# Optimization experiments

Hardware: AMD Instinct MI355X
Metric: run time of the kernel (lower is better)

The kernel has to match this reference:

```python
import jax, jax.numpy as jnp
import numpy as np

B, T, DE, DD, A, FN, FS = 32, 2000, 512, 1024, 128, 32, 16
TEMPERATURE = 1.0


def setup_inputs() -> dict:
    key = jax.random.key(0)
    ks = jax.random.split(key, 10)
    input_enc = jax.random.normal(ks[0], (B, T, DE), dtype=jnp.float32)
    # lengths in [T//2, T] so no zero-length utterances
    enc_lengths = jax.random.randint(ks[1], (B,), T // 2, T + 1, dtype=jnp.int32)
    input_dec = jax.random.normal(ks[2], (B, DD), dtype=jnp.float32)
    # prev_att: previous-step attention weights (masked, normalized)
    prev_att = jax.random.uniform(ks[3], (B, T), dtype=jnp.float32)
    pad = jnp.arange(T)[None, :] >= enc_lengths[:, None]
    prev_att = jnp.where(pad, 0.0, prev_att)
    prev_att = prev_att / jnp.sum(prev_att, axis=1, keepdims=True)
    # parameters
    conv_w = jax.random.normal(ks[4], (FN, 1, 2 * FS + 1), dtype=jnp.float32) * 0.1  # [out,in,k]
    enc_w = jax.random.normal(ks[5], (A, DE), dtype=jnp.float32) * 0.04
    dec_w = jax.random.normal(ks[6], (A, DD), dtype=jnp.float32) * 0.03
    att_w = jax.random.normal(ks[7], (A, FN), dtype=jnp.float32) * 0.17
    att_b = jnp.zeros((A,), dtype=jnp.float32)
    out_w = jax.random.normal(ks[8], (1, A), dtype=jnp.float32) * 0.09
    return dict(input_enc=input_enc, enc_lengths=enc_lengths, input_dec=input_dec,
                prev_att=prev_att, conv_w=conv_w, enc_w=enc_w, dec_w=dec_w,
                att_w=att_w, att_b=att_b, out_w=out_w)


def reference(input_enc, enc_lengths, input_dec, prev_att,
              conv_w, enc_w, dec_w, att_w, att_b, out_w):
    b, t, _ = input_enc.shape
    fs = (conv_w.shape[-1] - 1) // 2  # 'same' padding
    # padding mask: True at padded positions t >= length
    mask = jnp.arange(t)[None, :] >= enc_lengths[:, None]  # [B,T]
    # location features: Conv1d over prev attention, 1 -> FN channels, same length
    conv = jax.lax.conv_general_dilated(
        prev_att[:, None, :], conv_w, window_strides=(1,),
        padding=[(fs, fs)], dimension_numbers=("NCH", "OIH", "NCH"))  # [B,FN,T]
    loc_feat = conv.transpose(0, 2, 1)  # [B,T,FN]
    projected_att = loc_feat @ att_w.T + att_b        # [B,T,A]
    projected_enc = input_enc @ enc_w.T               # [B,T,A]
    projected_dec = (input_dec @ dec_w.T)[:, None, :]  # [B,1,A]
    score = jnp.squeeze(jnp.tanh(projected_att + projected_enc + projected_dec) @ out_w.T, -1)  # [B,T]
    score = jnp.where(mask, -jnp.inf, score)
    att_weight = jax.nn.softmax(TEMPERATURE * score, axis=1)  # [B,T]
    context = jnp.einsum("btd,bt->bd", input_enc, att_weight)  # [B,DE]
    return context, att_weight
```

## Files before the change

### kernel.cpp

```cpp
#include <hip/hip_runtime.h>
#include <hip/hip_bf16.h>
#include <math.h>

#define B_ 32
#define T_ 2000
#define DE_ 512
#define DD_ 1024
#define A_ 128
#define FN_ 32
#define FS_ 16
#define KW_ (2*FS_+1)

typedef __bf16 bf16x8 __attribute__((ext_vector_type(8)));
typedef __bf16 bf16x4 __attribute__((ext_vector_type(4)));
typedef float f32x4 __attribute__((ext_vector_type(4)));

#define BT 64
#define LSTR 40

__device__ __forceinline__ void load_lds16(const void* g, void* l) {
    __builtin_amdgcn_global_load_lds(
        (const __attribute__((address_space(1))) unsigned int*)g,
        (__attribute__((address_space(3))) unsigned int*)l, 16, 0, 0);
}

__global__ __launch_bounds__(256) void prep_kernel(
    const float* __restrict__ enc_w, const float* __restrict__ att_w,
    const float* __restrict__ input_dec, const float* __restrict__ dec_w,
    const float* __restrict__ att_b,
    __bf16* __restrict__ enc_bf, __bf16* __restrict__ att_bf,
    float* __restrict__ pdec)
{
    int bx = blockIdx.x, tid = threadIdx.x;
    if (bx < 64) {
        int i = bx * 256 + tid;
        float4 v = ((const float4*)enc_w)[i];
        bf16x4 o;
        o[0] = (__bf16)v.x; o[1] = (__bf16)v.y; o[2] = (__bf16)v.z; o[3] = (__bf16)v.w;
        *(bf16x4*)(enc_bf + (size_t)i * 4) = o;
        if (i < (A_ * FN_) / 4) {
            float4 w = ((const float4*)att_w)[i];
            bf16x4 p;
            p[0] = (__bf16)w.x; p[1] = (__bf16)w.y; p[2] = (__bf16)w.z; p[3] = (__bf16)w.w;
            *(bf16x4*)(att_bf + (size_t)i * 4) = p;
        }
    } else {
        int pb = bx - 64;
        int b  = pb >> 2;
        int a0 = (pb & 3) * 32;
        int al = tid >> 3;
        int kg = tid & 7;
        int a  = a0 + al;
        const float4* w = (const float4*)(dec_w + (size_t)a * DD_);
        const float4* x = (const float4*)(input_dec + (size_t)b * DD_);
        float acc = 0.f;
        #pragma unroll 8
        for (int j = 0; j < 32; j++) {
            int i4 = kg + j * 8;
            float4 wv = w[i4], xv = x[i4];
            acc += wv.x * xv.x + wv.y * xv.y + wv.z * xv.z + wv.w * xv.w;
        }
        acc += __shfl_xor(acc, 1, 64);
        acc += __shfl_xor(acc, 2, 64);
        acc += __shfl_xor(acc, 4, 64);
        if (kg == 0) pdec[b * A_ + a] = acc + att_b[a];
    }
}

__global__ __launch_bounds__(256, 4) void score_kernel(
    const float* __restrict__ input_enc, const __bf16* __restrict__ enc_bf,
    const float* __restrict__ prev_att,  const float* __restrict__ conv_w,
    const __bf16* __restrict__ att_bf,   const float* __restrict__ pdec,
    const float* __restrict__ out_w,     float* __restrict__ score)
{
    __shared__ __align__(16) char Bt[16384];
    __shared__ float pa_s[BT + 2 * FS_];
    __shared__ float cw_s[KW_ * FN_];
    __shared__ __align__(16) __bf16 loc_s[BT * LSTR];

    const int tid = threadIdx.x;
    const int b  = blockIdx.y;
    const int t0 = blockIdx.x * BT;

    for (int j = tid; j < BT + 2 * FS_; j += 256) {
        int t = t0 - FS_ + j;
        pa_s[j] = (t >= 0 && t < T_) ? prev_att[b * T_ + t] : 0.f;
    }
    for (int idx = tid; idx < FN_ * KW_; idx += 256) {
        int f = idx / KW_, k = idx % KW_;
        cw_s[k * FN_ + f] = conv_w[idx];
    }
    __syncthreads();

    {
        int f = tid & 31, r0 = tid >> 5;
        for (int r = r0; r < BT; r += 8) {
            float acc = 0.f;
            #pragma unroll
            for (int k = 0; k < KW_; k++) acc += pa_s[r + k] * cw_s[k * FN_ + f];
            loc_s[r * LSTR + f] = (__bf16)acc;
        }
    }
    __syncthreads();

    const int lane = tid & 63;
    const int wv   = tid >> 6;
    const int col  = lane & 15;
    const int grp  = lane >> 4;
    const int rowb = wv * 16 + col;
    const int t_row = t0 + rowb;
    const int t_clamp = t_row < T_ ? t_row : T_ - 1;
    const int sw = (col & 7);

    f32x4 acc[8];
    const f32x4 zero = (f32x4){0.f, 0.f, 0.f, 0.f};

    {
        bf16x8 afrag = *(const bf16x8*)(loc_s + rowb * LSTR + grp * 8);
        #pragma unroll
        for (int i = 0; i < 8; i++) {
            bf16x8 bfrag = *(const bf16x8*)(att_bf + (size_t)(i * 16 + col) * FN_ + grp * 8);
            acc[i] = __builtin_amdgcn_mfma_f32_16x16x32_bf16(afrag, bfrag, zero, 0, 0, 0);
        }
    }

    const float* arow = input_enc + ((size_t)(b * T_ + t_clamp)) * DE_ + grp * 8;

    for (int kc = 0; kc < DE_; kc += 64) {
        #pragma unroll
        for (int j = 0; j < 4; j++) {
            int s  = j * 256 + tid;
            int r  = s >> 3;
            int cp = s & 7;
            int c  = cp ^ (r & 7);
            load_lds16(enc_bf + (size_t)r * DE_ + kc + c * 8,
                       Bt + j * 4096 + wv * 1024);
        }
        float4 a00 = *(const float4*)(arow + kc);
        float4 a01 = *(const float4*)(arow + kc + 4);
        float4 a10 = *(const float4*)(arow + kc + 32);
        float4 a11 = *(const float4*)(arow + kc + 36);
        __syncthreads();

        bf16x8 af;
        af[0] = (__bf16)a00.x; af[1] = (__bf16)a00.y;
        af[2] = (__bf16)a00.z; af[3] = (__bf16)a00.w;
        af[4] = (__bf16)a01.x; af[5] = (__bf16)a01.y;
        af[6] = (__bf16)a01.z; af[7] = (__bf16)a01.w;
        #pragma unroll
        for (int i = 0; i < 8; i++) {
            bf16x8 bfrag = *(const bf16x8*)(Bt + (i * 16 + col) * 128 + ((grp ^ sw) * 16));
            acc[i] = __builtin_amdgcn_mfma_f32_16x16x32_bf16(af, bfrag, acc[i], 0, 0, 0);
        }
        af[0] = (__bf16)a10.x; af[1] = (__bf16)a10.y;
        af[2] = (__bf16)a10.z; af[3] = (__bf16)a10.w;
        af[4] = (__bf16)a11.x; af[5] = (__bf16)a11.y;
        af[6] = (__bf16)a11.z; af[7] = (__bf16)a11.w;
        #pragma unroll
        for (int i = 0; i < 8; i++) {
            bf16x8 bfrag = *(const bf16x8*)(Bt + (i * 16 + col) * 128 + (((4 + grp) ^ sw) * 16));
            acc[i] = __builtin_amdgcn_mfma_f32_16x16x32_bf16(af, bfrag, acc[i], 0, 0, 0);
        }
        __syncthreads();
    }

    float s[4] = {0.f, 0.f, 0.f, 0.f};
    #pragma unroll
    for (int i = 0; i < 8; i++) {
        int a = i * 16 + col;
        float ow = out_w[a];
        float bias = pdec[b * A_ + a];
        #pragma unroll
        for (int r = 0; r < 4; r++) {
            float v = acc[i][r] + bias;
            v = fminf(fmaxf(v, -15.f), 15.f);
            float e = __expf(2.f * v);
            s[r] += ow * ((e - 1.f) / (e + 1.f));
        }
    }
    #pragma unroll
    for (int r = 0; r < 4; r++) {
        s[r] += __shfl_xor(s[r], 1, 64);
        s[r] += __shfl_xor(s[r], 2, 64);
        s[r] += __shfl_xor(s[r], 4, 64);
        s[r] += __shfl_xor(s[r], 8, 64);
    }
    if (col == 0) {
        #pragma unroll
        for (int r = 0; r < 4; r++) {
            int t = t0 + wv * 16 + grp * 4 + r;
            if (t < T_) score[b * T_ + t] = s[r];
        }
    }
}

__global__ __launch_bounds__(256) void smax_kernel(
    const float* __restrict__ score, const int* __restrict__ lengths,
    float* __restrict__ minv, float* __restrict__ ctx)
{
    int b = blockIdx.x;
    int tid = threadIdx.x;
    if (tid < 128)
        *(float4*)(ctx + b * DE_ + tid * 4) = make_float4(0.f, 0.f, 0.f, 0.f);
    int len = lengths[b];
    __shared__ float redm[4], reds[4];

    float m = -1e30f;
    for (int t = tid; t < T_; t += 256)
        if (t < len) m = fmaxf(m, score[b * T_ + t]);
    #pragma unroll
    for (int off = 1; off < 64; off <<= 1) m = fmaxf(m, __shfl_xor(m, off, 64));
    if ((tid & 63) == 0) redm[tid >> 6] = m;
    __syncthreads();
    m = fmaxf(fmaxf(redm[0], redm[1]), fmaxf(redm[2], redm[3]));

    float sum = 0.f;
    for (int t = tid; t < T_; t += 256)
        if (t < len) sum += __expf(score[b * T_ + t] - m);
    #pragma unroll
    for (int off = 1; off < 64; off <<= 1) sum += __shfl_xor(sum, off, 64);
    if ((tid & 63) == 0) reds[tid >> 6] = sum;
    __syncthreads();
    if (tid == 0) {
        sum = reds[0] + reds[1] + reds[2] + reds[3];
        minv[2 * b] = m;
        minv[2 * b + 1] = 1.f / sum;
    }
}

#define NCH 32
#define CCH 63
__global__ __launch_bounds__(256) void context_kernel(
    const float* __restrict__ enc, const float* __restrict__ score,
    const float* __restrict__ minv, const int* __restrict__ lengths,
    float* __restrict__ att, float* __restrict__ ctx)
{
    int b = blockIdx.y;
    int tstart = blockIdx.x * CCH;
    int len = lengths[b];
    float m = minv[2 * b], inv = minv[2 * b + 1];
    __shared__ float w_s[CCH];
    for (int j = threadIdx.x; j < CCH; j += 256) {
        int t = tstart + j;
        float w = 0.f;
        if (t < len) w = __expf(score[b * T_ + t] - m) * inv;
        if (t < T_) att[b * T_ + t] = w;
        w_s[j] = w;
    }
    __syncthreads();

    int tend = tstart + CCH < len ? tstart + CCH : len;
    if (tstart >= tend) return;
    int n = tend - tstart;
    int half = threadIdx.x >> 7;
    int d0 = (threadIdx.x & 127) * 4;
    const float* base = enc + ((size_t)(b * T_ + tstart)) * DE_ + d0;
    float ax = 0.f, ay = 0.f, az = 0.f, aw = 0.f;
    #pragma unroll 4
    for (int t = half; t < n; t += 2) {
        float w = w_s[t];
        float4 v = *(const float4*)(base + (size_t)t * DE_);
        ax += w * v.x; ay += w * v.y; az += w * v.z; aw += w * v.w;
    }
    atomicAdd(&ctx[b * DE_ + d0 + 0], ax);
    atomicAdd(&ctx[b * DE_ + d0 + 1], ay);
    atomicAdd(&ctx[b * DE_ + d0 + 2], az);
    atomicAdd(&ctx[b * DE_ + d0 + 3], aw);
}

extern "C" void kernel_launch(void* const* d_in, const int* in_sizes, int n_in,
                              void* d_out, int out_size, void* d_ws, size_t ws_size,
                              hipStream_t stream)
{
    const float* input_enc   = (const float*)d_in[0];
    const int*   enc_lengths = (const int*)d_in[1];
    const float* input_dec   = (const float*)d_in[2];
    const float* prev_att    = (const float*)d_in[3];
    const float* conv_w      = (const float*)d_in[4];
    const float* enc_w       = (const float*)d_in[5];
    const float* dec_w       = (const float*)d_in[6];
    const float* att_w       = (const float*)d_in[7];
    const float* att_b       = (const float*)d_in[8];
    const float* out_w       = (const float*)d_in[9];

    float* out = (float*)d_out;
    char* ws = (char*)d_ws;
    float*  pdec   = (float*)ws;
    float*  score  = (float*)(ws + 16384);
    __bf16* enc_bf = (__bf16*)(ws + 16384 + 256000);
    __bf16* att_bf = (__bf16*)(ws + 16384 + 256000 + 131072);
    float*  minv   = pdec;

    prep_kernel<<<192, 256, 0, stream>>>(enc_w, att_w, input_dec, dec_w, att_b,
                                         enc_bf, att_bf, pdec);

    dim3 sgrid((T_ + BT - 1) / BT, B_);
    score_kernel<<<sgrid, 256, 0, stream>>>(input_enc, enc_bf, prev_att, conv_w,
                                            att_bf, pdec, out_w, score);

    smax_kernel<<<B_, 256, 0, stream>>>(score, enc_lengths, minv, out);

    dim3 cgrid(NCH, B_);
    context_kernel<<<cgrid, 256, 0, stream>>>(input_enc, score, minv, enc_lengths,
                                              out + B_ * DE_, out);
}
```

Measured before the change: 245.8 us.

## Fuse softmax and context into score kernel using fixed bound shift

The score kernel now computes exp(score - sum|out_w|) directly, using the bound on tanh outputs as a static max in place of a separate max pass. In the same kernel it accumulates the unnormalized context from the enc tile it just loaded and atomically adds the partial denominators. A small finalize kernel then normalizes the weights and the context. This drops the separate softmax and context kernels and the second full read of input_enc, at the cost of more atomics and a possible loss of precision or underflow if scores sit far below the bound.

```diff
diff --git a/kernel.cpp b/kernel.cpp
--- a/kernel.cpp
+++ b/kernel.cpp
@@ -29,7 +29,7 @@
     const float* __restrict__ input_dec, const float* __restrict__ dec_w,
     const float* __restrict__ att_b,
     __bf16* __restrict__ enc_bf, __bf16* __restrict__ att_bf,
-    float* __restrict__ pdec)
+    float* __restrict__ pdec, float* __restrict__ ctx_un )
 {
     int bx = blockIdx.x, tid = threadIdx.x;
     if (bx < 64) {
@@ -44,7 +44,7 @@
             p[0] = (__bf16)w.x; p[1] = (__bf16)w.y; p[2] = (__bf16)w.z; p[3] = (__bf16)w.w;
             *(bf16x4*)(att_bf + (size_t)i * 4) = p;
         }
-    } else {
+    } else if (bx < 192) {
         int pb = bx - 64;
         int b  = pb >> 2;
         int a0 = (pb & 3) * 32;
@@ -64,6 +64,10 @@
         acc += __shfl_xor(acc, 2, 64);
         acc += __shfl_xor(acc, 4, 64);
         if (kg == 0) pdec[b * A_ + a] = acc + att_b[a];
+    } else {
+        int idx = (bx - 192) * 256 + tid;
+        if (idx < (B_ * DE_ + B_) / 4 + 1)
+            ((float4*)ctx_un)[idx] = make_float4(0.f, 0.f, 0.f, 0.f);
     }
 }
 
@@ -71,16 +75,20 @@
     const float* __restrict__ input_enc, const __bf16* __restrict__ enc_bf,
     const float* __restrict__ prev_att,  const float* __restrict__ conv_w,
     const __bf16* __restrict__ att_bf,   const float* __restrict__ pdec,
-    const float* __restrict__ out_w,     float* __restrict__ score)
+    const float* __restrict__ out_w,     const int* __restrict__ lengths,
+    float* __restrict__ wbuf, float* __restrict__ ctx_un,
+    float* __restrict__ denom)
 {
     __shared__ __align__(16) char Bt[16384];
     __shared__ float pa_s[BT + 2 * FS_];
     __shared__ float cw_s[KW_ * FN_];
     __shared__ __align__(16) __bf16 loc_s[BT * LSTR];
+    __shared__ float w_s[BT];
 
     const int tid = threadIdx.x;
     const int b  = blockIdx.y;
     const int t0 = blockIdx.x * BT;
+    const int len = lengths[b];
 
     for (int j = tid; j < BT + 2 * FS_; j += 256) {
         int t = t0 - FS_ + j;
@@ -165,10 +173,12 @@
     }
 
     float s[4] = {0.f, 0.f, 0.f, 0.f};
+    float Mabs = 0.f;
     #pragma unroll
     for (int i = 0; i < 8; i++) {
         int a = i * 16 + col;
         float ow = out_w[a];
+        Mabs += fabsf(ow);
         float bias = pdec[b * A_ + a];
         #pragma unroll
         for (int r = 0; r < 4; r++) {
@@ -185,87 +195,75 @@
         s[r] += __shfl_xor(s[r], 4, 64);
         s[r] += __shfl_xor(s[r], 8, 64);
     }
+    Mabs += __shfl_xor(Mabs, 1, 64);
+    Mabs += __shfl_xor(Mabs, 2, 64);
+    Mabs += __shfl_xor(Mabs, 4, 64);
+    Mabs += __shfl_xor(Mabs, 8, 64);
+
     if (col == 0) {
         #pragma unroll
         for (int r = 0; r < 4; r++) {
-            int t = t0 + wv * 16 + grp * 4 + r;
-            if (t < T_) score[b * T_ + t] = s[r];
-        }
-    }
-}
-
-__global__ __launch_bounds__(256) void smax_kernel(
-    const float* __restrict__ score, const int* __restrict__ lengths,
-    float* __restrict__ minv, float* __restrict__ ctx)
+            int rl = wv * 16 + grp * 4 + r;
+            int t = t0 + rl;
+            float w = 0.f;
+            if (t < len) w = __expf(s[r] - Mabs);
+            w_s[rl] = w;
+            if (t < T_) wbuf[b * T_ + t] = w;
+        }
+    }
+    __syncthreads();
+
+    if (tid < 64) {
+        float w = w_s[tid];
+        w += __shfl_xor(w, 1, 64);
+        w += __shfl_xor(w, 2, 64);
+        w += __shfl_xor(w, 4, 64);
+        w += __shfl_xor(w, 8, 64);
+        w += __shfl_xor(w, 16, 64);
+        w += __shfl_xor(w, 32, 64);
+        if (tid == 0) atomicAdd(&denom[b], w);
+    }
+
+    int n_eff = len - t0;
+    if (n_eff > BT) n_eff = BT;
+    if (n_eff > 0) {
+        int d0 = tid * 2;
+        const float* ebase = input_enc + ((size_t)(b * T_ + t0)) * DE_ + d0;
+        float cx = 0.f, cy = 0.f;
+        #pragma unroll 8
+        for (int t = 0; t < n_eff; t++) {
+            float w = w_s[t];
+            float2 v = *(const float2*)(ebase + (size_t)t * DE_);
+            cx += w * v.x;
+            cy += w * v.y;
+        }
+        atomicAdd(&ctx_un[b * DE_ + d0 + 0], cx);
+        atomicAdd(&ctx_un[b * DE_ + d0 + 1], cy);
+    }
+}
+
+__global__ __launch_bounds__(256) void finalize_kernel(
+    const float* __restrict__ wbuf, const float* __restrict__ ctx_un,
+    const float* __restrict__ denom, float* __restrict__ out)
 {
-    int b = blockIdx.x;
-    int tid = threadIdx.x;
-    if (tid < 128)
-        *(float4*)(ctx + b * DE_ + tid * 4) = make_float4(0.f, 0.f, 0.f, 0.f);
-    int len = lengths[b];
-    __shared__ float redm[4], reds[4];
-
-    float m = -1e30f;
-    for (int t = tid; t < T_; t += 256)
-        if (t < len) m = fmaxf(m, score[b * T_ + t]);
-    #pragma unroll
-    for (int off = 1; off < 64; off <<= 1) m = fmaxf(m, __shfl_xor(m, off, 64));
-    if ((tid & 63) == 0) redm[tid >> 6] = m;
-    __syncthreads();
-    m = fmaxf(fmaxf(redm[0], redm[1]), fmaxf(redm[2], redm[3]));
-
-    float sum = 0.f;
-    for (int t = tid; t < T_; t += 256)
-        if (t < len) sum += __expf(score[b * T_ + t] - m);
-    #pragma unroll
-    for (int off = 1; off < 64; off <<= 1) sum += __shfl_xor(sum, off, 64);
-    if ((tid & 63) == 0) reds[tid >> 6] = sum;
-    __syncthreads();
-    if (tid == 0) {
-        sum = reds[0] + reds[1] + reds[2] + reds[3];
-        minv[2 * b] = m;
-        minv[2 * b + 1] = 1.f / sum;
-    }
-}
-
-#define NCH 32
-#define CCH 63
-__global__ __launch_bounds__(256) void context_kernel(
-    const float* __restrict__ enc, const float* __restrict__ score,
-    const float* __restrict__ minv, const int* __restrict__ lengths,
-    float* __restrict__ att, float* __restrict__ ctx)
-{
-    int b = blockIdx.y;
-    int tstart = blockIdx.x * CCH;
-    int len = lengths[b];
-    float m = minv[2 * b], inv = minv[2 * b + 1];
-    __shared__ float w_s[CCH];
-    for (int j = threadIdx.x; j < CCH; j += 256) {
-        int t = tstart + j;
-        float w = 0.f;
-        if (t < len) w = __expf(score[b * T_ + t] - m) * inv;
-        if (t < T_) att[b * T_ + t] = w;
-        w_s[j] = w;
-    }
-    __syncthreads();
-
-    int tend = tstart + CCH < len ? tstart + CCH : len;
-    if (tstart >= tend) return;
-    int n = tend - tstart;
-    int half = threadIdx.x >> 7;
-    int d0 = (threadIdx.x & 127) * 4;
-    const float* base = enc + ((size_t)(b * T_ + tstart)) * DE_ + d0;
-    float ax = 0.f, ay = 0.f, az = 0.f, aw = 0.f;
-    #pragma unroll 4
-    for (int t = half; t < n; t += 2) {
-        float w = w_s[t];
-        float4 v = *(const float4*)(base + (size_t)t * DE_);
-        ax += w * v.x; ay += w * v.y; az += w * v.z; aw += w * v.w;
-    }
-    atomicAdd(&ctx[b * DE_ + d0 + 0], ax);
-    atomicAdd(&ctx[b * DE_ + d0 + 1], ay);
-    atomicAdd(&ctx[b * DE_ + d0 + 2], az);
-    atomicAdd(&ctx[b * DE_ + d0 + 3], aw);
+    int bx = blockIdx.x, tid = threadIdx.x;
+    if (bx < 64) {
+        int i4 = bx * 256 + tid;
+        if (i4 < (B_ * T_) / 4) {
+            int b = i4 / (T_ / 4);
+            float inv = 1.f / denom[b];
+            float4 w = ((const float4*)wbuf)[i4];
+            w.x *= inv; w.y *= inv; w.z *= inv; w.w *= inv;
+            ((float4*)(out + B_ * DE_))[i4] = w;
+        }
+    } else {
+        int j = (bx - 64) * 256 + tid;
+        int b = j / (DE_ / 4);
+        float inv = 1.f / denom[b];
+        float4 c = ((const float4*)ctx_un)[j];
+        c.x *= inv; c.y *= inv; c.z *= inv; c.w *= inv;
+        ((float4*)out)[j] = c;
+    }
 }
 
 extern "C" void kernel_launch(void* const* d_in, const int* in_sizes, int n_in,
@@ -286,21 +284,19 @@
     float* out = (float*)d_out;
     char* ws = (char*)d_ws;
     float*  pdec   = (float*)ws;
-    float*  score  = (float*)(ws + 16384);
-    __bf16* enc_bf = (__bf16*)(ws + 16384 + 256000);
-    __bf16* att_bf = (__bf16*)(ws + 16384 + 256000 + 131072);
-    float*  minv   = pdec;
-
-    prep_kernel<<<192, 256, 0, stream>>>(enc_w, att_w, input_dec, dec_w, att_b,
-                                         enc_bf, att_bf, pdec);
+    float*  wbuf   = (float*)(ws + 16384);
+    __bf16* enc_bf = (__bf16*)(ws + 272384);
+    __bf16* att_bf = (__bf16*)(ws + 403456);
+    float*  ctx_un = (float*)(ws + 411648);
+    float*  denom  = (float*)(ws + 477184);
+
+    prep_kernel<<<209, 256, 0, stream>>>(enc_w, att_w, input_dec, dec_w, att_b,
+                                         enc_bf, att_bf, pdec, ctx_un);
 
     dim3 sgrid((T_ + BT - 1) / BT, B_);
     score_kernel<<<sgrid, 256, 0, stream>>>(input_enc, enc_bf, prev_att, conv_w,
-                                            att_bf, pdec, out_w, score);
-
-    smax_kernel<<<B_, 256, 0, stream>>>(score, enc_lengths, minv, out);
-
-    dim3 cgrid(NCH, B_);
-    context_kernel<<<cgrid, 256, 0, stream>>>(input_enc, score, minv, enc_lengths,
-                                              out + B_ * DE_, out);
-}
+                                            att_bf, pdec, out_w, enc_lengths,
+                                            wbuf, ctx_un, denom);
+
+    finalize_kernel<<<80, 256, 0, stream>>>(wbuf, ctx_un, denom, out);
+}
```

Result: faster. 225.9 us (-8.1%).
